# Kernel optimization log

Measured on AMD Instinct MI355X. Metric: run time of the kernel, lower is better.

The kernel has to match this reference:

```python
import jax, jax.numpy as jnp
import numpy as np

N = 50000
E = 800000
IN, HID, OUT = 64, 128, 64


def sage_conv(x, edge_index, W_l, b_l, W_r):
    # PyG SAGEConv (aggr='mean', root_weight=True):
    #   out = lin_l(mean_{j in N(i)} x_j) + lin_r(x_i)
    src, dst = edge_index[0], edge_index[1]
    msg = x[src]                                   # [E, d] gather
    agg = jax.ops.segment_sum(msg, dst, num_segments=x.shape[0])  # [N, d]
    cnt = jax.ops.segment_sum(jnp.ones((msg.shape[0],), x.dtype), dst,
                              num_segments=x.shape[0])
    mean = agg / jnp.maximum(cnt, 1.0)[:, None]
    return mean @ W_l + b_l + x @ W_r


def setup_inputs() -> dict:
    key = jax.random.key(0)
    ks = jax.random.split(key, 8)
    x = jax.random.normal(ks[0], (N, IN), dtype=jnp.float32)
    edge_index = jax.random.randint(ks[1], (2, E), 0, N, dtype=jnp.int64)
    s1 = 1.0 / np.sqrt(IN)
    s2 = 1.0 / np.sqrt(HID)
    W1_l = jax.random.uniform(ks[2], (IN, HID), jnp.float32, -s1, s1)
    W1_r = jax.random.uniform(ks[3], (IN, HID), jnp.float32, -s1, s1)
    b1 = jax.random.uniform(ks[4], (HID,), jnp.float32, -s1, s1)
    W2_l = jax.random.uniform(ks[5], (HID, OUT), jnp.float32, -s2, s2)
    W2_r = jax.random.uniform(ks[6], (HID, OUT), jnp.float32, -s2, s2)
    b2 = jax.random.uniform(ks[7], (OUT,), jnp.float32, -s2, s2)
    return {"x": x, "edge_index": edge_index,
            "W1_l": W1_l, "b1": b1, "W1_r": W1_r,
            "W2_l": W2_l, "b2": b2, "W2_r": W2_r}


def reference(x, edge_index, W1_l, b1, W1_r, W2_l, b2, W2_r):
    h = jax.nn.relu(sage_conv(x, edge_index, W1_l, b1, W1_r))
    return sage_conv(h, edge_index, W2_l, b2, W2_r)
```

## Files before the change

### kernel.cpp

```cpp
#include <hip/hip_runtime.h>


#define FMA4(acc, f, w0, w1, w2, w3)                          \
  acc.x += f.x * w0.x + f.y * w1.x + f.z * w2.x + f.w * w3.x; \
  acc.y += f.x * w0.y + f.y * w1.y + f.z * w2.y + f.w * w3.y; \
  acc.z += f.x * w0.z + f.y * w1.z + f.z * w2.z + f.w * w3.z; \
  acc.w += f.x * w0.w + f.y * w1.w + f.z * w2.w + f.w * w3.w;

__global__ __launch_bounds__(256) void k_hist(const int* __restrict__ dst,
                                              int* __restrict__ deg, int E) {
  int e = blockIdx.x * blockDim.x + threadIdx.x;
  if (e < E) atomicAdd(&deg[dst[e]], 1);
}

__global__ __launch_bounds__(256) void k_assign(const int* __restrict__ deg,
                                                int* __restrict__ rowptr,
                                                int* __restrict__ pos,
                                                int* __restrict__ total,
                                                int N) {
  int i = blockIdx.x * blockDim.x + threadIdx.x;
  if (i >= N) return;
  int r = atomicAdd(total, deg[i]);
  rowptr[i] = r;
  pos[i] = r;
}

__global__ __launch_bounds__(256) void k_fill(const int* __restrict__ src,
                                              const int* __restrict__ dst,
                                              int* __restrict__ pos,
                                              int* __restrict__ colsrc, int E) {
  int e = blockIdx.x * blockDim.x + threadIdx.x;
  if (e >= E) return;
  int slot = atomicAdd(&pos[dst[e]], 1);
  colsrc[slot] = src[e];
}

__global__ __launch_bounds__(256, 4) void k_layer1(
    const float* __restrict__ x, const int* __restrict__ rowptr,
    const int* __restrict__ deg, const int* __restrict__ colsrc,
    const float* __restrict__ W1l, const float* __restrict__ b1,
    const float* __restrict__ W1r, const float* __restrict__ W2l,
    const float* __restrict__ W2r, float* __restrict__ p,
    float* __restrict__ q, int N) {
  int i0 = blockIdx.x * 32;
  int tid = threadIdx.x;
  __shared__ float smem[32 * 132];
  float(*ms)[64] = (float(*)[64])smem;
  float(*xs)[64] = (float(*)[64])(smem + 32 * 64);
  float(*hs)[132] = (float(*)[132])smem;

  {
    int wv = tid >> 6;
    int ln = tid & 63;
    int eg = ln >> 4;
    int c4 = (ln & 15) << 2;
    for (int nn = 0; nn < 8; ++nn) {
      int n = wv * 8 + nn;
      int node = i0 + n;
      float4 s0 = make_float4(0.f, 0.f, 0.f, 0.f);
      float4 s1 = s0;
      int d = 0;
      if (node < N) {
        int beg = rowptr[node];
        d = deg[node];
        int end = beg + d;
        int e = beg + eg;
        for (; e + 4 < end; e += 8) {
          const float4 v0 = *reinterpret_cast<const float4*>(
              x + (size_t)colsrc[e] * 64 + c4);
          const float4 v1 = *reinterpret_cast<const float4*>(
              x + (size_t)colsrc[e + 4] * 64 + c4);
          s0.x += v0.x; s0.y += v0.y; s0.z += v0.z; s0.w += v0.w;
          s1.x += v1.x; s1.y += v1.y; s1.z += v1.z; s1.w += v1.w;
        }
        for (; e < end; e += 4) {
          const float4 v = *reinterpret_cast<const float4*>(
              x + (size_t)colsrc[e] * 64 + c4);
          s0.x += v.x; s0.y += v.y; s0.z += v.z; s0.w += v.w;
        }
      }
      s0.x += s1.x; s0.y += s1.y; s0.z += s1.z; s0.w += s1.w;
#pragma unroll
      for (int m = 16; m <= 32; m <<= 1) {
        s0.x += __shfl_xor(s0.x, m);
        s0.y += __shfl_xor(s0.y, m);
        s0.z += __shfl_xor(s0.z, m);
        s0.w += __shfl_xor(s0.w, m);
      }
      if (eg == 0) {
        float r = 1.f / fmaxf((float)d, 1.f);
        *(float4*)&ms[n][c4] =
            make_float4(s0.x * r, s0.y * r, s0.z * r, s0.w * r);
      }
    }
  }
  for (int t = tid; t < 512; t += 256) {
    int n = t >> 4;
    int c4 = (t & 15) << 2;
    int node = i0 + n;
    float4 zx = make_float4(0.f, 0.f, 0.f, 0.f);
    if (node < N) zx = *(const float4*)&x[(size_t)node * 64 + c4];
    *(float4*)&xs[n][c4] = zx;
  }
  __syncthreads();

  int jt = tid & 31;
  int j0 = jt << 2;
  int nt = tid >> 5;
  int n0 = nt << 2;
  float4 acc[4];
  {
    float4 bj = *(const float4*)&b1[j0];
    acc[0] = bj; acc[1] = bj; acc[2] = bj; acc[3] = bj;
  }
#pragma unroll 4
  for (int k0 = 0; k0 < 64; k0 += 4) {
    float4 wl[4], wr[4];
#pragma unroll
    for (int kk = 0; kk < 4; ++kk) {
      wl[kk] = *(const float4*)&W1l[(size_t)(k0 + kk) * 128 + j0];
      wr[kk] = *(const float4*)&W1r[(size_t)(k0 + kk) * 128 + j0];
    }
#pragma unroll
    for (int n = 0; n < 4; ++n) {
      float4 m4 = *(const float4*)&ms[n0 + n][k0];
      float4 x4 = *(const float4*)&xs[n0 + n][k0];
      FMA4(acc[n], m4, wl[0], wl[1], wl[2], wl[3]);
      FMA4(acc[n], x4, wr[0], wr[1], wr[2], wr[3]);
    }
  }
  __syncthreads();

#pragma unroll
  for (int n = 0; n < 4; ++n) {
    float4 v = acc[n];
    v.x = fmaxf(v.x, 0.f);
    v.y = fmaxf(v.y, 0.f);
    v.z = fmaxf(v.z, 0.f);
    v.w = fmaxf(v.w, 0.f);
    *(float4*)&hs[n0 + n][j0] = v;
  }
  __syncthreads();

  const float* W = (tid < 128) ? W2l : W2r;
  float* ob = (tid < 128) ? p : q;
  int t2 = tid & 127;
  int jj0 = (t2 & 15) << 2;
  int nn0 = (t2 >> 4) << 2;
  float4 pa[4];
  pa[0] = make_float4(0.f, 0.f, 0.f, 0.f);
  pa[1] = pa[0]; pa[2] = pa[0]; pa[3] = pa[0];
#pragma unroll 4
  for (int k0 = 0; k0 < 128; k0 += 4) {
    float4 w[4];
#pragma unroll
    for (int kk = 0; kk < 4; ++kk)
      w[kk] = *(const float4*)&W[(size_t)(k0 + kk) * 64 + jj0];
#pragma unroll
    for (int n = 0; n < 4; ++n) {
      float4 h4 = *(const float4*)&hs[nn0 + n][k0];
      FMA4(pa[n], h4, w[0], w[1], w[2], w[3]);
    }
  }
#pragma unroll
  for (int n = 0; n < 4; ++n) {
    int node = i0 + nn0 + n;
    if (node < N) *(float4*)&ob[(size_t)node * 64 + jj0] = pa[n];
  }
}

__global__ __launch_bounds__(256) void k_layer2(
    const float* __restrict__ p, const int* __restrict__ rowptr,
    const int* __restrict__ deg, const int* __restrict__ colsrc,
    const float* __restrict__ q, const float* __restrict__ b2,
    float* __restrict__ out, int N) {
  int wave = threadIdx.x >> 6;
  int lane = threadIdx.x & 63;
  int node = blockIdx.x * 4 + wave;
  if (node >= N) return;
  int beg = rowptr[node];
  int d = deg[node];
  int end = beg + d;
  int eg = lane >> 4;
  int c4 = (lane & 15) << 2;
  float4 s0 = make_float4(0.f, 0.f, 0.f, 0.f);
  float4 s1 = s0, s2 = s0, s3 = s0;
  int e = beg + eg;
  for (; e + 12 < end; e += 16) {
    const float4 v0 =
        *reinterpret_cast<const float4*>(p + (size_t)colsrc[e] * 64 + c4);
    const float4 v1 =
        *reinterpret_cast<const float4*>(p + (size_t)colsrc[e + 4] * 64 + c4);
    const float4 v2 =
        *reinterpret_cast<const float4*>(p + (size_t)colsrc[e + 8] * 64 + c4);
    const float4 v3 =
        *reinterpret_cast<const float4*>(p + (size_t)colsrc[e + 12] * 64 + c4);
    s0.x += v0.x; s0.y += v0.y; s0.z += v0.z; s0.w += v0.w;
    s1.x += v1.x; s1.y += v1.y; s1.z += v1.z; s1.w += v1.w;
    s2.x += v2.x; s2.y += v2.y; s2.z += v2.z; s2.w += v2.w;
    s3.x += v3.x; s3.y += v3.y; s3.z += v3.z; s3.w += v3.w;
  }
  for (; e < end; e += 4) {
    const float4 v =
        *reinterpret_cast<const float4*>(p + (size_t)colsrc[e] * 64 + c4);
    s0.x += v.x; s0.y += v.y; s0.z += v.z; s0.w += v.w;
  }
  s0.x += s1.x + s2.x + s3.x;
  s0.y += s1.y + s2.y + s3.y;
  s0.z += s1.z + s2.z + s3.z;
  s0.w += s1.w + s2.w + s3.w;
#pragma unroll
  for (int m = 16; m <= 32; m <<= 1) {
    s0.x += __shfl_xor(s0.x, m);
    s0.y += __shfl_xor(s0.y, m);
    s0.z += __shfl_xor(s0.z, m);
    s0.w += __shfl_xor(s0.w, m);
  }
  if (eg == 0) {
    float r = 1.f / fmaxf((float)d, 1.f);
    float4 a = *(const float4*)&q[(size_t)node * 64 + c4];
    float4 b = *(const float4*)&b2[c4];
    float4 o = make_float4(s0.x * r + a.x + b.x, s0.y * r + a.y + b.y,
                           s0.z * r + a.z + b.z, s0.w * r + a.w + b.w);
    *reinterpret_cast<float4*>(out + (size_t)node * 64 + c4) = o;
  }
}

extern "C" void kernel_launch(void* const* d_in, const int* in_sizes, int n_in,
                              void* d_out, int out_size, void* d_ws,
                              size_t ws_size, hipStream_t stream) {
  const float* x = (const float*)d_in[0];
  const int* ei = (const int*)d_in[1];
  const float* W1l = (const float*)d_in[2];
  const float* b1 = (const float*)d_in[3];
  const float* W1r = (const float*)d_in[4];
  const float* W2l = (const float*)d_in[5];
  const float* b2 = (const float*)d_in[6];
  const float* W2r = (const float*)d_in[7];
  float* out = (float*)d_out;

  const int N = in_sizes[0] / 64;
  const int E = in_sizes[1] / 2;
  const int* src = ei;
  const int* dst = ei + E;

  int* deg = (int*)d_ws;
  int* total = deg + N;
  int* rowptr = total + 1;
  int* pos = rowptr + N;
  int* colsrc = pos + N;
  float* p = (float*)(colsrc + E);
  float* q = p + (size_t)N * 64;

  hipMemsetAsync(deg, 0, (size_t)(N + 1) * sizeof(int), stream);
  k_hist<<<(E + 255) / 256, 256, 0, stream>>>(dst, deg, E);
  k_assign<<<(N + 255) / 256, 256, 0, stream>>>(deg, rowptr, pos, total, N);
  k_fill<<<(E + 255) / 256, 256, 0, stream>>>(src, dst, pos, colsrc, E);

  int nblk32 = (N + 31) / 32;
  int nblk4 = (N + 3) / 4;
  k_layer1<<<nblk32, 256, 0, stream>>>(x, rowptr, deg, colsrc, W1l, b1, W1r,
                                       W2l, W2r, p, q, N);
  k_layer2<<<nblk4, 256, 0, stream>>>(p, rowptr, deg, colsrc, q, b2, out, N);
}
```

Before: 327.4 us.

## Pad CSR rows to 4, gather with int4 indices, one 16-lane group per node

```diff
diff --git a/kernel.cpp b/kernel.cpp
--- a/kernel.cpp
+++ b/kernel.cpp
@@ -20,7 +20,8 @@
                                                 int N) {
   int i = blockIdx.x * blockDim.x + threadIdx.x;
   if (i >= N) return;
-  int r = atomicAdd(total, deg[i]);
+  int d4 = (deg[i] + 3) & ~3;
+  int r = atomicAdd(total, d4);
   rowptr[i] = r;
   pos[i] = r;
 }
@@ -42,59 +43,61 @@
     const float* __restrict__ W1r, const float* __restrict__ W2l,
     const float* __restrict__ W2r, float* __restrict__ p,
     float* __restrict__ q, int N) {
-  int i0 = blockIdx.x * 32;
+  int i0 = blockIdx.x * 64;
   int tid = threadIdx.x;
-  __shared__ float smem[32 * 132];
-  float(*ms)[64] = (float(*)[64])smem;
-  float(*xs)[64] = (float(*)[64])(smem + 32 * 64);
+  __shared__ float smem[64 * 68 * 2];
+  float(*ms)[68] = (float(*)[68])smem;
+  float(*xs)[68] = (float(*)[68])(smem + 64 * 68);
   float(*hs)[132] = (float(*)[132])smem;
 
   {
-    int wv = tid >> 6;
-    int ln = tid & 63;
-    int eg = ln >> 4;
-    int c4 = (ln & 15) << 2;
-    for (int nn = 0; nn < 8; ++nn) {
-      int n = wv * 8 + nn;
-      int node = i0 + n;
+    int grp = tid >> 4;
+    int c4 = (tid & 15) << 2;
+    for (int nn = 0; nn < 4; ++nn) {
+      int nl = grp * 4 + nn;
+      int node = i0 + nl;
       float4 s0 = make_float4(0.f, 0.f, 0.f, 0.f);
-      float4 s1 = s0;
-      int d = 0;
+      float4 s1 = s0, s2 = s0, s3 = s0;
+      float rd = 0.f;
       if (node < N) {
-        int beg = rowptr[node];
-        d = deg[node];
-        int end = beg + d;
-        int e = beg + eg;
-        for (; e + 4 < end; e += 8) {
-          const float4 v0 = *reinterpret_cast<const float4*>(
-              x + (size_t)colsrc[e] * 64 + c4);
-          const float4 v1 = *reinterpret_cast<const float4*>(
-              x + (size_t)colsrc[e + 4] * 64 + c4);
+        int base = rowptr[node];
+        int d = deg[node];
+        rd = 1.f / fmaxf((float)d, 1.f);
+        int i = 0;
+        for (; i + 8 <= d; i += 8) {
+          int4 ia = *(const int4*)&colsrc[base + i];
+          int4 ib = *(const int4*)&colsrc[base + i + 4];
+          float4 v0 = *(const float4*)&x[(size_t)ia.x * 64 + c4];
+          float4 v1 = *(const float4*)&x[(size_t)ia.y * 64 + c4];
+          float4 v2 = *(const float4*)&x[(size_t)ia.z * 64 + c4];
+          float4 v3 = *(const float4*)&x[(size_t)ia.w * 64 + c4];
+          float4 v4 = *(const float4*)&x[(size_t)ib.x * 64 + c4];
+          float4 v5 = *(const float4*)&x[(size_t)ib.y * 64 + c4];
+          float4 v6 = *(const float4*)&x[(size_t)ib.z * 64 + c4];
+          float4 v7 = *(const float4*)&x[(size_t)ib.w * 64 + c4];
           s0.x += v0.x; s0.y += v0.y; s0.z += v0.z; s0.w += v0.w;
           s1.x += v1.x; s1.y += v1.y; s1.z += v1.z; s1.w += v1.w;
+          s2.x += v2.x; s2.y += v2.y; s2.z += v2.z; s2.w += v2.w;
+          s3.x += v3.x; s3.y += v3.y; s3.z += v3.z; s3.w += v3.w;
+          s0.x += v4.x; s0.y += v4.y; s0.z += v4.z; s0.w += v4.w;
+          s1.x += v5.x; s1.y += v5.y; s1.z += v5.z; s1.w += v5.w;
+          s2.x += v6.x; s2.y += v6.y; s2.z += v6.z; s2.w += v6.w;
+          s3.x += v7.x; s3.y += v7.y; s3.z += v7.z; s3.w += v7.w;
         }
-        for (; e < end; e += 4) {
-          const float4 v = *reinterpret_cast<const float4*>(
-              x + (size_t)colsrc[e] * 64 + c4);
+        for (; i < d; ++i) {
+          int idx = colsrc[base + i];
+          float4 v = *(const float4*)&x[(size_t)idx * 64 + c4];
           s0.x += v.x; s0.y += v.y; s0.z += v.z; s0.w += v.w;
         }
       }
-      s0.x += s1.x; s0.y += s1.y; s0.z += s1.z; s0.w += s1.w;
-#pragma unroll
-      for (int m = 16; m <= 32; m <<= 1) {
-        s0.x += __shfl_xor(s0.x, m);
-        s0.y += __shfl_xor(s0.y, m);
-        s0.z += __shfl_xor(s0.z, m);
-        s0.w += __shfl_xor(s0.w, m);
-      }
-      if (eg == 0) {
-        float r = 1.f / fmaxf((float)d, 1.f);
-        *(float4*)&ms[n][c4] =
-            make_float4(s0.x * r, s0.y * r, s0.z * r, s0.w * r);
-      }
-    }
-  }
-  for (int t = tid; t < 512; t += 256) {
+      s0.x = (s0.x + s1.x + s2.x + s3.x) * rd;
+      s0.y = (s0.y + s1.y + s2.y + s3.y) * rd;
+      s0.z = (s0.z + s1.z + s2.z + s3.z) * rd;
+      s0.w = (s0.w + s1.w + s2.w + s3.w) * rd;
+      *(float4*)&ms[nl][c4] = s0;
+    }
+  }
+  for (int t = tid; t < 1024; t += 256) {
     int n = t >> 4;
     int c4 = (t & 15) << 2;
     int node = i0 + n;
@@ -107,13 +110,14 @@
   int jt = tid & 31;
   int j0 = jt << 2;
   int nt = tid >> 5;
-  int n0 = nt << 2;
-  float4 acc[4];
+  int n0 = nt << 3;
+  float4 acc[8];
   {
     float4 bj = *(const float4*)&b1[j0];
-    acc[0] = bj; acc[1] = bj; acc[2] = bj; acc[3] = bj;
-  }
-#pragma unroll 4
+#pragma unroll
+    for (int n = 0; n < 8; ++n) acc[n] = bj;
+  }
+#pragma unroll 2
   for (int k0 = 0; k0 < 64; k0 += 4) {
     float4 wl[4], wr[4];
 #pragma unroll
@@ -122,7 +126,7 @@
       wr[kk] = *(const float4*)&W1r[(size_t)(k0 + kk) * 128 + j0];
     }
 #pragma unroll
-    for (int n = 0; n < 4; ++n) {
+    for (int n = 0; n < 8; ++n) {
       float4 m4 = *(const float4*)&ms[n0 + n][k0];
       float4 x4 = *(const float4*)&xs[n0 + n][k0];
       FMA4(acc[n], m4, wl[0], wl[1], wl[2], wl[3]);
@@ -132,7 +136,7 @@
   __syncthreads();
 
 #pragma unroll
-  for (int n = 0; n < 4; ++n) {
+  for (int n = 0; n < 8; ++n) {
     float4 v = acc[n];
     v.x = fmaxf(v.x, 0.f);
     v.y = fmaxf(v.y, 0.f);
@@ -146,26 +150,26 @@
   float* ob = (tid < 128) ? p : q;
   int t2 = tid & 127;
   int jj0 = (t2 & 15) << 2;
-  int nn0 = (t2 >> 4) << 2;
-  float4 pa[4];
-  pa[0] = make_float4(0.f, 0.f, 0.f, 0.f);
-  pa[1] = pa[0]; pa[2] = pa[0]; pa[3] = pa[0];
-#pragma unroll 4
+  int g2 = t2 >> 4;
+  float4 pa[8];
+#pragma unroll
+  for (int n = 0; n < 8; ++n) pa[n] = make_float4(0.f, 0.f, 0.f, 0.f);
+#pragma unroll 2
   for (int k0 = 0; k0 < 128; k0 += 4) {
     float4 w[4];
 #pragma unroll
     for (int kk = 0; kk < 4; ++kk)
       w[kk] = *(const float4*)&W[(size_t)(k0 + kk) * 64 + jj0];
 #pragma unroll
-    for (int n = 0; n < 4; ++n) {
-      float4 h4 = *(const float4*)&hs[nn0 + n][k0];
-      FMA4(pa[n], h4, w[0], w[1], w[2], w[3]);
-    }
-  }
-#pragma unroll
-  for (int n = 0; n < 4; ++n) {
-    int node = i0 + nn0 + n;
-    if (node < N) *(float4*)&ob[(size_t)node * 64 + jj0] = pa[n];
+    for (int m = 0; m < 8; ++m) {
+      float4 h4 = *(const float4*)&hs[g2 + 8 * m][k0];
+      FMA4(pa[m], h4, w[0], w[1], w[2], w[3]);
+    }
+  }
+#pragma unroll
+  for (int m = 0; m < 8; ++m) {
+    int node = i0 + g2 + 8 * m;
+    if (node < N) *(float4*)&ob[(size_t)node * 64 + jj0] = pa[m];
   }
 }
 
@@ -174,56 +178,48 @@
     const int* __restrict__ deg, const int* __restrict__ colsrc,
     const float* __restrict__ q, const float* __restrict__ b2,
     float* __restrict__ out, int N) {
-  int wave = threadIdx.x >> 6;
-  int lane = threadIdx.x & 63;
-  int node = blockIdx.x * 4 + wave;
+  int node = blockIdx.x * 16 + (threadIdx.x >> 4);
   if (node >= N) return;
-  int beg = rowptr[node];
+  int c4 = (threadIdx.x & 15) << 2;
+  int base = rowptr[node];
   int d = deg[node];
-  int end = beg + d;
-  int eg = lane >> 4;
-  int c4 = (lane & 15) << 2;
   float4 s0 = make_float4(0.f, 0.f, 0.f, 0.f);
   float4 s1 = s0, s2 = s0, s3 = s0;
-  int e = beg + eg;
-  for (; e + 12 < end; e += 16) {
-    const float4 v0 =
-        *reinterpret_cast<const float4*>(p + (size_t)colsrc[e] * 64 + c4);
-    const float4 v1 =
-        *reinterpret_cast<const float4*>(p + (size_t)colsrc[e + 4] * 64 + c4);
-    const float4 v2 =
-        *reinterpret_cast<const float4*>(p + (size_t)colsrc[e + 8] * 64 + c4);
-    const float4 v3 =
-        *reinterpret_cast<const float4*>(p + (size_t)colsrc[e + 12] * 64 + c4);
+  int i = 0;
+  for (; i + 8 <= d; i += 8) {
+    int4 ia = *(const int4*)&colsrc[base + i];
+    int4 ib = *(const int4*)&colsrc[base + i + 4];
+    float4 v0 = *(const float4*)&p[(size_t)ia.x * 64 + c4];
+    float4 v1 = *(const float4*)&p[(size_t)ia.y * 64 + c4];
+    float4 v2 = *(const float4*)&p[(size_t)ia.z * 64 + c4];
+    float4 v3 = *(const float4*)&p[(size_t)ia.w * 64 + c4];
+    float4 v4 = *(const float4*)&p[(size_t)ib.x * 64 + c4];
+    float4 v5 = *(const float4*)&p[(size_t)ib.y * 64 + c4];
+    float4 v6 = *(const float4*)&p[(size_t)ib.z * 64 + c4];
+    float4 v7 = *(const float4*)&p[(size_t)ib.w * 64 + c4];
     s0.x += v0.x; s0.y += v0.y; s0.z += v0.z; s0.w += v0.w;
     s1.x += v1.x; s1.y += v1.y; s1.z += v1.z; s1.w += v1.w;
     s2.x += v2.x; s2.y += v2.y; s2.z += v2.z; s2.w += v2.w;
     s3.x += v3.x; s3.y += v3.y; s3.z += v3.z; s3.w += v3.w;
-  }
-  for (; e < end; e += 4) {
-    const float4 v =
-        *reinterpret_cast<const float4*>(p + (size_t)colsrc[e] * 64 + c4);
+    s0.x += v4.x; s0.y += v4.y; s0.z += v4.z; s0.w += v4.w;
+    s1.x += v5.x; s1.y += v5.y; s1.z += v5.z; s1.w += v5.w;
+    s2.x += v6.x; s2.y += v6.y; s2.z += v6.z; s2.w += v6.w;
+    s3.x += v7.x; s3.y += v7.y; s3.z += v7.z; s3.w += v7.w;
+  }
+  for (; i < d; ++i) {
+    int idx = colsrc[base + i];
+    float4 v = *(const float4*)&p[(size_t)idx * 64 + c4];
     s0.x += v.x; s0.y += v.y; s0.z += v.z; s0.w += v.w;
   }
-  s0.x += s1.x + s2.x + s3.x;
-  s0.y += s1.y + s2.y + s3.y;
-  s0.z += s1.z + s2.z + s3.z;
-  s0.w += s1.w + s2.w + s3.w;
-#pragma unroll
-  for (int m = 16; m <= 32; m <<= 1) {
-    s0.x += __shfl_xor(s0.x, m);
-    s0.y += __shfl_xor(s0.y, m);
-    s0.z += __shfl_xor(s0.z, m);
-    s0.w += __shfl_xor(s0.w, m);
-  }
-  if (eg == 0) {
-    float r = 1.f / fmaxf((float)d, 1.f);
-    float4 a = *(const float4*)&q[(size_t)node * 64 + c4];
-    float4 b = *(const float4*)&b2[c4];
-    float4 o = make_float4(s0.x * r + a.x + b.x, s0.y * r + a.y + b.y,
-                           s0.z * r + a.z + b.z, s0.w * r + a.w + b.w);
-    *reinterpret_cast<float4*>(out + (size_t)node * 64 + c4) = o;
-  }
+  float r = 1.f / fmaxf((float)d, 1.f);
+  float4 a = *(const float4*)&q[(size_t)node * 64 + c4];
+  float4 b = *(const float4*)&b2[c4];
+  float4 o;
+  o.x = (s0.x + s1.x + s2.x + s3.x) * r + a.x + b.x;
+  o.y = (s0.y + s1.y + s2.y + s3.y) * r + a.y + b.y;
+  o.z = (s0.z + s1.z + s2.z + s3.z) * r + a.z + b.z;
+  o.w = (s0.w + s1.w + s2.w + s3.w) * r + a.w + b.w;
+  *(float4*)&out[(size_t)node * 64 + c4] = o;
 }
 
 extern "C" void kernel_launch(void* const* d_in, const int* in_sizes, int n_in,
@@ -249,7 +245,7 @@
   int* rowptr = total + 1;
   int* pos = rowptr + N;
   int* colsrc = pos + N;
-  float* p = (float*)(colsrc + E);
+  float* p = (float*)(colsrc + (E + 4 * N));
   float* q = p + (size_t)N * 64;
 
   hipMemsetAsync(deg, 0, (size_t)(N + 1) * sizeof(int), stream);
@@ -257,9 +253,9 @@
   k_assign<<<(N + 255) / 256, 256, 0, stream>>>(deg, rowptr, pos, total, N);
   k_fill<<<(E + 255) / 256, 256, 0, stream>>>(src, dst, pos, colsrc, E);
 
-  int nblk32 = (N + 31) / 32;
-  int nblk4 = (N + 3) / 4;
-  k_layer1<<<nblk32, 256, 0, stream>>>(x, rowptr, deg, colsrc, W1l, b1, W1r,
+  int nblk64 = (N + 63) / 64;
+  int nblk16 = (N + 15) / 16;
+  k_layer1<<<nblk64, 256, 0, stream>>>(x, rowptr, deg, colsrc, W1l, b1, W1r,
                                        W2l, W2r, p, q, N);
-  k_layer2<<<nblk4, 256, 0, stream>>>(p, rowptr, deg, colsrc, q, b2, out, N);
-}
+  k_layer2<<<nblk16, 256, 0, stream>>>(p, rowptr, deg, colsrc, q, b2, out, N);
+}
```

Result: slower. 360.8 us (+10.2%).
